# Optimization experiments

Hardware: AMD Instinct MI355X
Metric: run time of the kernel (lower is better)

## Reference

```python
import jax, jax.numpy as jnp
import numpy as np

NP, NR, NK = 64, 8, 500          # problems, rollouts, candidate nodes
H, HEADS, VD = 256, 8, 8         # hidden_dim, heads, vars_dim
HD = H // HEADS                  # head_dim
CLIP = 10.0                      # tanh logit clipping
NEG_INF = -jnp.inf


def setup_inputs() -> dict:
    key = jax.random.key(0)
    ks = jax.random.split(key, 17)
    f = lambda k, s: jax.random.normal(k, s, dtype=jnp.float32)
    B = NP * NR
    s = 1.0 / np.sqrt(H)
    return {
        "X": f(ks[0], (NP, NK, H)),
        "K": f(ks[1], (HEADS, NP, NK, HD)),
        "V": f(ks[2], (HEADS, NP, NK, HD)),
        "query": f(ks[3], (B, H)),
        "state1": f(ks[4], (B, H)),
        "state2": f(ks[5], (B, H)),
        "varfeat": f(ks[6], (NP, VD, NK)),
        "mask": jax.random.uniform(ks[7], (NP, NR, NK)) < 0.1,
        "nn_Q": f(ks[8], (HEADS, H, HD)) * (1.0 / np.sqrt(HD)),
        "nn_O": f(ks[9], (H, H)) * s,
        "nn_A": f(ks[10], (VD, H)) * s,
        "nn_B": f(ks[11], (H,)) * s,
        "nn_W": f(ks[12], (H,)) * s,
        "W_ih": f(ks[13], (4 * H, H)) * s,
        "W_hh": f(ks[14], (4 * H, H)) * s,
        "b_ih": f(ks[15], (4 * H,)) * s,
        "b_hh": f(ks[16], (4 * H,)) * s,
    }


def _decode(X, K, V, query, state1, state2, varfeat, mask,
            nn_Q, nn_O, nn_A, nn_B, nn_W, W_ih, W_hh, b_ih, b_hh):
    B = query.shape[0]
    # --- LSTMCell (PyTorch gate order: i, f, g, o) ---
    gates = query @ W_ih.T + b_ih + state1 @ W_hh.T + b_hh
    i, fg, g, o = jnp.split(gates, 4, axis=1)
    c = jax.nn.sigmoid(fg) * state2 + jax.nn.sigmoid(i) * jnp.tanh(g)
    h = jax.nn.sigmoid(o) * jnp.tanh(c)
    # --- MultiHeadAttention (glimpse) ---
    q = h.reshape(NP, NR, H)
    Q = jnp.einsum('pqh,ahd->apqd', q, nn_Q)                    # [heads,NP,NR,HD]
    S = jnp.einsum('apqd,apkd->apqk', Q, K) * (1.0 / np.sqrt(HD))
    S = jnp.where(mask[None], NEG_INF, S)
    S = jax.nn.softmax(S, axis=-1)
    x = jnp.einsum('apqk,apkd->apqd', S, V)
    x = x.transpose(1, 2, 0, 3).reshape(NP, NR, H)              # [NP,NR,H]
    qm = x @ nn_O                                               # glimpse query
    # --- additive attention with variable features ---
    vf = jnp.einsum('pvk,vh->pkh', varfeat, nn_A) + nn_B        # [NP,NK,H]
    t = jnp.tanh(X[:, None] + vf[:, None] + qm[:, :, None])     # [NP,NR,NK,H]
    logit = jnp.einsum('pqkh,h->pqk', t, nn_W)
    logit = jnp.where(mask, NEG_INF, logit).reshape(B, NK)
    # --- choose (mode=1: greedy argmax) ---
    infeasible = logit == NEG_INF
    l = jnp.where(infeasible, NEG_INF, jnp.tanh(logit) * CLIP)
    chosen = jnp.argmax(l, axis=1)
    logp = jax.nn.log_softmax(l, axis=1)
    chosen_p = jnp.take_along_axis(logp, chosen[:, None], axis=1).squeeze(1)
    return h, c, chosen_p


def reference(X, K, V, query, state1, state2, varfeat, mask,
              nn_Q, nn_O, nn_A, nn_B, nn_W, W_ih, W_hh, b_ih, b_hh):
    return _decode(X, K, V, query, state1, state2, varfeat, mask,
                   nn_Q, nn_O, nn_A, nn_B, nn_W, W_ih, W_hh, b_ih, b_hh)
```

## Files before the change

kernel.cpp:

```cpp
#include <hip/hip_runtime.h>

#define NPP   64
#define NRR   8
#define NKK   500
#define HDIM  256
#define NHEAD 8
#define VDIM  8
#define HD    32
#define BTOT  512

__device__ __forceinline__ float fast_tanh(float x) {
  const float e = __expf(2.f * x);
  return 1.f - 2.f * __builtin_amdgcn_rcpf(e + 1.f);
}
__device__ __forceinline__ float fast_sig(float x) {
  return __builtin_amdgcn_rcpf(1.f + __expf(-x));
}

__global__ __launch_bounds__(64) void k_lstm4(
    const float* __restrict__ query, const float* __restrict__ state1,
    const float* __restrict__ state2,
    const float* __restrict__ W_ih, const float* __restrict__ W_hh,
    const float* __restrict__ b_ih, const float* __restrict__ b_hh,
    const unsigned char* __restrict__ maskb, int* __restrict__ flagp,
    float* __restrict__ out_h, float* __restrict__ out_c)
{
  __shared__ float Wt[32][40];
  __shared__ float At[32][40];
  __shared__ float gt[32][40];

  const int t  = threadIdx.x;
  const int hb = blockIdx.x;
  const int bb = blockIdx.y;

  if (flagp != nullptr && hb == 0 && bb == 0) {
    __shared__ int f;
    if (t == 0) f = 0;
    __syncthreads();
    int any = 0;
    for (int j = t; j < 2048; j += 64) any |= maskb[2 * j + 1];
    if (any) atomicOr(&f, 1);
    __syncthreads();
    if (t == 0) *flagp = f;
  }

  const int tr = t >> 3, tc = t & 7;
  const int srow = t >> 1, sseg = (t & 1) * 16;
  const int wgrow = (srow >> 3) * HDIM + hb * 8 + (srow & 7);
  const int agrow = bb * 32 + srow;

  float acc[4][4];
#pragma unroll
  for (int i = 0; i < 4; ++i)
#pragma unroll
    for (int j = 0; j < 4; ++j) acc[i][j] = 0.f;

  for (int k0 = 0; k0 < 512; k0 += 32) {
    __syncthreads();
    {
      const float* wsrc = (k0 < 256) ? (W_ih + (size_t)wgrow * HDIM + k0)
                                     : (W_hh + (size_t)wgrow * HDIM + (k0 - 256));
      const float* asrc = (k0 < 256) ? (query  + (size_t)agrow * HDIM + k0)
                                     : (state1 + (size_t)agrow * HDIM + (k0 - 256));
#pragma unroll
      for (int j = 0; j < 4; ++j) {
        const float4 wv = *reinterpret_cast<const float4*>(wsrc + sseg + 4 * j);
        const float4 av = *reinterpret_cast<const float4*>(asrc + sseg + 4 * j);
        const int kk = sseg + 4 * j;
        Wt[kk + 0][srow] = wv.x; Wt[kk + 1][srow] = wv.y;
        Wt[kk + 2][srow] = wv.z; Wt[kk + 3][srow] = wv.w;
        At[kk + 0][srow] = av.x; At[kk + 1][srow] = av.y;
        At[kk + 2][srow] = av.z; At[kk + 3][srow] = av.w;
      }
    }
    __syncthreads();
#pragma unroll 8
    for (int kk = 0; kk < 32; ++kk) {
      const float4 wv = *reinterpret_cast<const float4*>(&Wt[kk][tr * 4]);
      const float4 av = *reinterpret_cast<const float4*>(&At[kk][tc * 4]);
      const float w[4] = {wv.x, wv.y, wv.z, wv.w};
      const float a[4] = {av.x, av.y, av.z, av.w};
#pragma unroll
      for (int i = 0; i < 4; ++i)
#pragma unroll
        for (int j = 0; j < 4; ++j) acc[i][j] += w[i] * a[j];
    }
  }

#pragma unroll
  for (int i = 0; i < 4; ++i) {
    float4 v;
    v.x = acc[i][0]; v.y = acc[i][1]; v.z = acc[i][2]; v.w = acc[i][3];
    *reinterpret_cast<float4*>(&gt[tr * 4 + i][tc * 4]) = v;
  }
  __syncthreads();

#pragma unroll
  for (int it = 0; it < 4; ++it) {
    const int cell = t + 64 * it;
    const int b = cell & 31, h = cell >> 5;
    const int gh = hb * 8 + h;
    const int gb = bb * 32 + b;
    const float bi = b_ih[0 * HDIM + gh] + b_hh[0 * HDIM + gh];
    const float bf = b_ih[1 * HDIM + gh] + b_hh[1 * HDIM + gh];
    const float bg = b_ih[2 * HDIM + gh] + b_hh[2 * HDIM + gh];
    const float bo = b_ih[3 * HDIM + gh] + b_hh[3 * HDIM + gh];
    const float iv = fast_sig (gt[ 0 + h][b] + bi);
    const float fv = fast_sig (gt[ 8 + h][b] + bf);
    const float gv = fast_tanh(gt[16 + h][b] + bg);
    const float ov = fast_sig (gt[24 + h][b] + bo);
    const size_t off = (size_t)gb * HDIM + gh;
    const float c = fv * state2[off] + iv * gv;
    out_c[off] = c;
    out_h[off] = ov * fast_tanh(c);
  }
}

__global__ __launch_bounds__(512, 4) void k_attn8(
    const float* __restrict__ Kt, const float* __restrict__ Vt,
    const float* __restrict__ nn_Q, const float* __restrict__ nn_O,
    const void* __restrict__ maskp, const int* __restrict__ flagp,
    const float* __restrict__ out_h, float* __restrict__ qm_slabs)
{
  const int p = blockIdx.x >> 3;
  const int a = blockIdx.x & 7;
  const int t = threadIdx.x;
  const int wave = t >> 6, lane = t & 63;

  __shared__ float hs[NRR][HDIM];
  __shared__ float Qs[NRR][36];
  __shared__ float Sb[NRR][512];
  __shared__ float pb[16][NRR][HD];
  __shared__ float xs[NRR][36];

  const float4 hv = reinterpret_cast<const float4*>(
      out_h + (size_t)p * NRR * HDIM)[t];

  const int flag = *flagp;

  const int kc = (t < NKK) ? t : (NKK - 1);
  const float4* kp4 = reinterpret_cast<const float4*>(
      Kt + (((size_t)a * NPP + p) * NKK + kc) * HD);
  float4 kreg[8];
#pragma unroll
  for (int j = 0; j < 8; ++j) kreg[j] = kp4[j];

  const int dpv = t & 31, kb = t >> 5;
  const float* vb = Vt + (((size_t)a * NPP + p) * NKK + (size_t)kb * 32) * HD + dpv;
  float vreg[32];
#pragma unroll
  for (int j = 0; j < 32; ++j)
    vreg[j] = (kb * 32 + j < NKK) ? vb[(size_t)j * HD] : 0.f;

  float maskv[NRR];
  {
    const unsigned char* mb = (const unsigned char*)maskp;
    const int* mi = (const int*)maskp;
#pragma unroll
    for (int r = 0; r < NRR; ++r) {
      const size_t mo = (size_t)(p * NRR + r) * NKK + kc;
      const bool mk = flag ? (mb[mo] != 0) : (mi[mo] != 0);
      maskv[r] = mk ? -INFINITY : 0.f;
    }
  }

  reinterpret_cast<float4*>(&hs[0][0])[t] = hv;
  __syncthreads();

  {
    const int r = wave, d4 = lane >> 3, ks = lane & 7;
    const float* qb = nn_Q + ((size_t)a * HDIM + ks * 32) * HD + d4 * 4;
    float qx = 0.f, qy = 0.f, qz = 0.f, qw = 0.f;
#pragma unroll
    for (int h = 0; h < 32; ++h) {
      const float hval = hs[r][ks * 32 + h];
      const float4 wv = *reinterpret_cast<const float4*>(qb + (size_t)h * HD);
      qx += hval * wv.x; qy += hval * wv.y;
      qz += hval * wv.z; qw += hval * wv.w;
    }
#pragma unroll
    for (int off = 1; off < 8; off <<= 1) {
      qx += __shfl_xor(qx, off, 64);
      qy += __shfl_xor(qy, off, 64);
      qz += __shfl_xor(qz, off, 64);
      qw += __shfl_xor(qw, off, 64);
    }
    if (ks == 0) {
      const float sc = 0.17677669529663687f;
      Qs[r][d4 * 4 + 0] = qx * sc; Qs[r][d4 * 4 + 1] = qy * sc;
      Qs[r][d4 * 4 + 2] = qz * sc; Qs[r][d4 * 4 + 3] = qw * sc;
    }
  }
  __syncthreads();

#pragma unroll
  for (int r = 0; r < NRR; ++r) {
    float s = 0.f;
#pragma unroll
    for (int j = 0; j < 8; ++j) {
      const float4 q = *reinterpret_cast<const float4*>(&Qs[r][j * 4]);
      const float4 k4 = kreg[j];
      s += q.x * k4.x + q.y * k4.y + q.z * k4.z + q.w * k4.w;
    }
    Sb[r][t] = (t < NKK) ? (s + maskv[r]) : -INFINITY;
  }
  __syncthreads();

  {
    const int r = wave;
    float lv[8], m = -INFINITY;
#pragma unroll
    for (int i = 0; i < 8; ++i) {
      lv[i] = Sb[r][lane + 64 * i];
      m = fmaxf(m, lv[i]);
    }
#pragma unroll
    for (int off = 32; off > 0; off >>= 1) m = fmaxf(m, __shfl_xor(m, off, 64));
    float ssum = 0.f;
#pragma unroll
    for (int i = 0; i < 8; ++i) {
      lv[i] = __expf(lv[i] - m);
      ssum += lv[i];
    }
#pragma unroll
    for (int off = 32; off > 0; off >>= 1) ssum += __shfl_xor(ssum, off, 64);
    const float inv = 1.f / ssum;
#pragma unroll
    for (int i = 0; i < 8; ++i) Sb[r][lane + 64 * i] = lv[i] * inv;
  }
  __syncthreads();

  {
    float acc[NRR];
#pragma unroll
    for (int r = 0; r < NRR; ++r) acc[r] = 0.f;
#pragma unroll
    for (int j4 = 0; j4 < 8; ++j4) {
      const float v0 = vreg[j4 * 4 + 0], v1 = vreg[j4 * 4 + 1];
      const float v2 = vreg[j4 * 4 + 2], v3 = vreg[j4 * 4 + 3];
#pragma unroll
      for (int r = 0; r < NRR; ++r) {
        const float4 s4 = *reinterpret_cast<const float4*>(
            &Sb[r][kb * 32 + j4 * 4]);
        acc[r] += s4.x * v0 + s4.y * v1 + s4.z * v2 + s4.w * v3;
      }
    }
#pragma unroll
    for (int r = 0; r < NRR; ++r) pb[kb][r][dpv] = acc[r];
  }
  __syncthreads();

  if (t < 256) {
    const int r = t >> 5, d = t & 31;
    float s = 0.f;
#pragma unroll
    for (int q = 0; q < 16; ++q) s += pb[q][r][d];
    xs[r][d] = s;
  }
  __syncthreads();

  {
    const int j = t & 255, rr = t >> 8;
    float a0 = 0.f, a1 = 0.f, a2 = 0.f, a3 = 0.f;
#pragma unroll
    for (int d4 = 0; d4 < 8; ++d4) {
      const float4 x0 = *reinterpret_cast<const float4*>(&xs[rr * 4 + 0][d4 * 4]);
      const float4 x1 = *reinterpret_cast<const float4*>(&xs[rr * 4 + 1][d4 * 4]);
      const float4 x2 = *reinterpret_cast<const float4*>(&xs[rr * 4 + 2][d4 * 4]);
      const float4 x3 = *reinterpret_cast<const float4*>(&xs[rr * 4 + 3][d4 * 4]);
      const float c0[4] = {x0.x, x0.y, x0.z, x0.w};
      const float c1[4] = {x1.x, x1.y, x1.z, x1.w};
      const float c2[4] = {x2.x, x2.y, x2.z, x2.w};
      const float c3[4] = {x3.x, x3.y, x3.z, x3.w};
#pragma unroll
      for (int dd = 0; dd < 4; ++dd) {
        const float w = nn_O[((size_t)(a * HD + d4 * 4 + dd)) * HDIM + j];
        a0 += c0[dd] * w; a1 += c1[dd] * w;
        a2 += c2[dd] * w; a3 += c3[dd] * w;
      }
    }
    float* slab = qm_slabs + (size_t)a * BTOT * HDIM;
    slab[(size_t)(p * NRR + rr * 4 + 0) * HDIM + j] = a0;
    slab[(size_t)(p * NRR + rr * 4 + 1) * HDIM + j] = a1;
    slab[(size_t)(p * NRR + rr * 4 + 2) * HDIM + j] = a2;
    slab[(size_t)(p * NRR + rr * 4 + 3) * HDIM + j] = a3;
  }
}

__global__ __launch_bounds__(256) void k_logits6(
    const float* __restrict__ X, const float* __restrict__ varfeat,
    const float* __restrict__ nn_A, const float* __restrict__ nn_B,
    const float* __restrict__ nn_W, const float* __restrict__ qm_slabs,
    const int* __restrict__ flagp, const void* __restrict__ maskp,
    float* __restrict__ pmax, float* __restrict__ psum)
{
  const int p  = blockIdx.x >> 5;
  const int kt = blockIdx.x & 31;
  const int t = threadIdx.x;
  const int wave = t >> 6, lane = t & 63;
  const int h0 = lane * 4;

  __shared__ float qb[NRR][260];
  __shared__ float red[4][NRR][2];

  const unsigned char* mb = (const unsigned char*)maskp;
  const int* mi = (const int*)maskp;
  const int flag = *flagp;
  const bool mbyte = (flag != 0);

  for (int s = t; s < 512; s += 256) {
    const int r = s >> 6, h4 = s & 63;
    const float4 bv = *reinterpret_cast<const float4*>(nn_B + h4 * 4);
    float qx = bv.x, qy = bv.y, qz = bv.z, qw = bv.w;
#pragma unroll
    for (int a = 0; a < NHEAD; ++a) {
      const float4 q = *reinterpret_cast<const float4*>(
          qm_slabs + (size_t)a * BTOT * HDIM +
          (size_t)(p * NRR + r) * HDIM + h4 * 4);
      qx += q.x; qy += q.y; qz += q.z; qw += q.w;
    }
    qb[r][h4 * 4 + 0] = qx; qb[r][h4 * 4 + 1] = qy;
    qb[r][h4 * 4 + 2] = qz; qb[r][h4 * 4 + 3] = qw;
  }
  __syncthreads();

  const float4 w4 = *reinterpret_cast<const float4*>(nn_W + h0);
  float4 a4r[VDIM];
#pragma unroll
  for (int v = 0; v < VDIM; ++v)
    a4r[v] = *reinterpret_cast<const float4*>(nn_A + (size_t)v * HDIM + h0);
  float4 q4r[NRR];
#pragma unroll
  for (int r = 0; r < NRR; ++r)
    q4r[r] = *reinterpret_cast<const float4*>(&qb[r][h0]);

  float rmax = -INFINITY, rsum = 0.f;

  for (int kk = 0; kk < 4; ++kk) {
    const int k = kt * 16 + wave * 4 + kk;
    if (k >= NKK) break;

    const float4 x4 = *reinterpret_cast<const float4*>(
        X + ((size_t)p * NKK + k) * HDIM + h0);
    float base0 = x4.x, base1 = x4.y, base2 = x4.z, base3 = x4.w;
#pragma unroll
    for (int v = 0; v < VDIM; ++v) {
      const float vv = varfeat[((size_t)p * VDIM + v) * NKK + k];
      base0 += vv * a4r[v].x; base1 += vv * a4r[v].y;
      base2 += vv * a4r[v].z; base3 += vv * a4r[v].w;
    }

    float acc[NRR];
#pragma unroll
    for (int r = 0; r < NRR; ++r) {
      acc[r] = fast_tanh(base0 + q4r[r].x) * w4.x
             + fast_tanh(base1 + q4r[r].y) * w4.y
             + fast_tanh(base2 + q4r[r].z) * w4.z
             + fast_tanh(base3 + q4r[r].w) * w4.w;
    }

    float v4[4];
    {
      float sw[8];
#pragma unroll
      for (int j = 0; j < 8; ++j) sw[j] = __shfl_xor(acc[j], 32, 64);
      const bool hi = (lane & 32) != 0;
#pragma unroll
      for (int j = 0; j < 4; ++j)
        v4[j] = hi ? (acc[j + 4] + sw[j + 4]) : (acc[j] + sw[j]);
    }
    float v2[2];
    {
      float sw[4];
#pragma unroll
      for (int j = 0; j < 4; ++j) sw[j] = __shfl_xor(v4[j], 16, 64);
      const bool hi = (lane & 16) != 0;
      v2[0] = hi ? (v4[2] + sw[2]) : (v4[0] + sw[0]);
      v2[1] = hi ? (v4[3] + sw[3]) : (v4[1] + sw[1]);
    }
    float w;
    {
      const float s0 = __shfl_xor(v2[0], 8, 64);
      const float s1 = __shfl_xor(v2[1], 8, 64);
      w = ((lane & 8) != 0) ? (v2[1] + s1) : (v2[0] + s0);
    }
    w += __shfl_xor(w, 4, 64);
    w += __shfl_xor(w, 2, 64);
    w += __shfl_xor(w, 1, 64);

    if ((lane & 7) == 0) {
      const int r = lane >> 3;
      const size_t mrow = (size_t)(p * NRR + r) * NKK + k;
      const bool mk = mbyte ? (mb[mrow] != 0) : (mi[mrow] != 0);
      const float l = mk ? -INFINITY : fast_tanh(w) * 10.0f;
      rmax = fmaxf(rmax, l);
      rsum += __expf(l - 10.f);
    }
  }

  if ((lane & 7) == 0) {
    red[wave][lane >> 3][0] = rmax;
    red[wave][lane >> 3][1] = rsum;
  }
  __syncthreads();
  if (t < NRR) {
    float m = red[0][t][0], s = red[0][t][1];
#pragma unroll
    for (int w = 1; w < 4; ++w) {
      m = fmaxf(m, red[w][t][0]);
      s += red[w][t][1];
    }
    pmax[(size_t)(p * NRR + t) * 32 + kt] = m;
    psum[(size_t)(p * NRR + t) * 32 + kt] = s;
  }
}

__global__ __launch_bounds__(64) void k_choose2(
    const float* __restrict__ pmax, const float* __restrict__ psum,
    float* __restrict__ out_p)
{
  const int b = blockIdx.x;
  const int lane = threadIdx.x;
  float m = (lane < 32) ? pmax[(size_t)b * 32 + lane] : -INFINITY;
  float s = (lane < 32) ? psum[(size_t)b * 32 + lane] : 0.f;
#pragma unroll
  for (int off = 16; off > 0; off >>= 1) {
    m = fmaxf(m, __shfl_xor(m, off, 64));
    s += __shfl_xor(s, off, 64);
  }
  if (lane == 0) out_p[b] = m - 10.f - logf(s);
}

__global__ __launch_bounds__(256) void k_fused(
    const float* __restrict__ X, const float* __restrict__ Kt,
    const float* __restrict__ Vt, const float* __restrict__ varfeat,
    const void* __restrict__ maskp,
    const float* __restrict__ nn_Q, const float* __restrict__ nn_O,
    const float* __restrict__ nn_A, const float* __restrict__ nn_B,
    const float* __restrict__ nn_W,
    const float* __restrict__ out_h, float* __restrict__ out_p)
{
  const int p = blockIdx.x >> 3;
  const int r = blockIdx.x & 7;
  const int t = threadIdx.x;
  const int wave = t >> 6, lane = t & 63;

  __shared__ float hs[HDIM];
  __shared__ float Qs[NHEAD][HD];
  __shared__ float Sb[NHEAD][NKK];
  __shared__ float xs[HDIM];
  __shared__ float qs[HDIM];
  __shared__ float As2[HDIM][VDIM];
  __shared__ float Ws[HDIM];
  __shared__ float lsb[NKK];
  __shared__ int   mask_any;

  const unsigned char* mb = (const unsigned char*)maskp;
  if (t == 0) mask_any = 0;
  __syncthreads();
  {
    int any = 0;
    for (int j = t; j < 2048; j += 256) any |= mb[2 * j + 1];
    if (any) atomicOr(&mask_any, 1);
  }
  for (int idx = t; idx < VDIM * HDIM; idx += 256)
    As2[idx & 255][idx >> 8] = nn_A[idx];
  Ws[t] = nn_W[t];
  hs[t] = out_h[(size_t)(p * NRR + r) * HDIM + t];
  __syncthreads();
  const bool mbyte = (mask_any != 0);
  const int* mi = (const int*)maskp;
  const size_t mrow = (size_t)(p * NRR + r) * NKK;
  {
    const int a = t >> 5, d = t & 31;
    const float* nq = nn_Q + (size_t)a * HDIM * HD + d;
    float acc = 0.f;
    for (int h = 0; h < HDIM; ++h) acc += hs[h] * nq[(size_t)h * HD];
    Qs[a][d] = acc * 0.17677669529663687f;
  }
  __syncthreads();
  for (int k = t; k < NKK; k += 256) {
    const bool mk = mbyte ? (mb[mrow + k] != 0) : (mi[mrow + k] != 0);
#pragma unroll
    for (int a = 0; a < NHEAD; ++a) {
      const float4* kr4 = reinterpret_cast<const float4*>(
          Kt + (((size_t)a * NPP + p) * NKK + k) * HD);
      float s = 0.f;
#pragma unroll
      for (int d4 = 0; d4 < HD / 4; ++d4) {
        const float4 u = kr4[d4];
        s += Qs[a][4 * d4] * u.x + Qs[a][4 * d4 + 1] * u.y
           + Qs[a][4 * d4 + 2] * u.z + Qs[a][4 * d4 + 3] * u.w;
      }
      Sb[a][k] = mk ? -INFINITY : s;
    }
  }
  __syncthreads();
  for (int aa = 0; aa < 2; ++aa) {
    const int a = wave * 2 + aa;
    float m = -INFINITY;
    for (int k = lane; k < NKK; k += 64) m = fmaxf(m, Sb[a][k]);
#pragma unroll
    for (int off = 32; off > 0; off >>= 1) m = fmaxf(m, __shfl_xor(m, off, 64));
    float ssum = 0.f;
    for (int k = lane; k < NKK; k += 64) {
      const float e = expf(Sb[a][k] - m);
      Sb[a][k] = e; ssum += e;
    }
#pragma unroll
    for (int off = 32; off > 0; off >>= 1) ssum += __shfl_xor(ssum, off, 64);
    const float inv = 1.f / ssum;
    for (int k = lane; k < NKK; k += 64) Sb[a][k] *= inv;
  }
  __syncthreads();
  {
    const int a = t >> 5, d = t & 31;
    const float* vb = Vt + ((size_t)a * NPP + p) * NKK * HD + d;
    float acc = 0.f;
    for (int k = 0; k < NKK; ++k) acc += Sb[a][k] * vb[(size_t)k * HD];
    xs[a * HD + d] = acc;
  }
  __syncthreads();
  {
    float acc = 0.f;
    for (int i = 0; i < HDIM; ++i) acc += xs[i] * nn_O[(size_t)i * HDIM + t];
    qs[t] = acc + nn_B[t];
  }
  __syncthreads();
  for (int k = t; k < NKK; k += 256) {
    float vfv[VDIM];
#pragma unroll
    for (int v = 0; v < VDIM; ++v)
      vfv[v] = varfeat[((size_t)p * VDIM + v) * NKK + k];
    const float4* xp4 = reinterpret_cast<const float4*>(
        X + ((size_t)p * NKK + k) * HDIM);
    float acc = 0.f;
    for (int h4 = 0; h4 < HDIM / 4; ++h4) {
      const float4 ux = xp4[h4];
      const float xv[4] = {ux.x, ux.y, ux.z, ux.w};
#pragma unroll
      for (int j = 0; j < 4; ++j) {
        const int h = 4 * h4 + j;
        float base = xv[j] + qs[h];
        const float4 a0 = *reinterpret_cast<const float4*>(&As2[h][0]);
        const float4 a1 = *reinterpret_cast<const float4*>(&As2[h][4]);
        base += vfv[0] * a0.x + vfv[1] * a0.y + vfv[2] * a0.z + vfv[3] * a0.w
              + vfv[4] * a1.x + vfv[5] * a1.y + vfv[6] * a1.z + vfv[7] * a1.w;
        acc += tanhf(base) * Ws[h];
      }
    }
    lsb[k] = acc;
  }
  __syncthreads();
  for (int k = t; k < NKK; k += 256) {
    const bool mk = mbyte ? (mb[mrow + k] != 0) : (mi[mrow + k] != 0);
    lsb[k] = mk ? -INFINITY : tanhf(lsb[k]) * 10.0f;
  }
  __syncthreads();
  if (wave == 0) {
    float m = -INFINITY;
    for (int k = lane; k < NKK; k += 64) m = fmaxf(m, lsb[k]);
#pragma unroll
    for (int off = 32; off > 0; off >>= 1) m = fmaxf(m, __shfl_xor(m, off, 64));
    float s = 0.f;
    for (int k = lane; k < NKK; k += 64) s += expf(lsb[k] - m);
#pragma unroll
    for (int off = 32; off > 0; off >>= 1) s += __shfl_xor(s, off, 64);
    if (lane == 0) out_p[p * NRR + r] = -logf(s);
  }
}

extern "C" void kernel_launch(void* const* d_in, const int* in_sizes, int n_in,
                              void* d_out, int out_size, void* d_ws, size_t ws_size,
                              hipStream_t stream)
{
  const float* X       = (const float*)d_in[0];
  const float* Kt      = (const float*)d_in[1];
  const float* Vt      = (const float*)d_in[2];
  const float* query   = (const float*)d_in[3];
  const float* state1  = (const float*)d_in[4];
  const float* state2  = (const float*)d_in[5];
  const float* varfeat = (const float*)d_in[6];
  const void*  maskp   = d_in[7];
  const float* nn_Q    = (const float*)d_in[8];
  const float* nn_O    = (const float*)d_in[9];
  const float* nn_A    = (const float*)d_in[10];
  const float* nn_B    = (const float*)d_in[11];
  const float* nn_W    = (const float*)d_in[12];
  const float* W_ih    = (const float*)d_in[13];
  const float* W_hh    = (const float*)d_in[14];
  const float* b_ih    = (const float*)d_in[15];
  const float* b_hh    = (const float*)d_in[16];

  float* out   = (float*)d_out;
  float* out_h = out;
  float* out_c = out + (size_t)BTOT * HDIM;
  float* out_p = out + (size_t)2 * BTOT * HDIM;

  const size_t flag_bytes = 256;
  const size_t qm8_bytes  = (size_t)NHEAD * BTOT * HDIM * 4;
  const size_t part_bytes = (size_t)BTOT * 32 * 4;
  const size_t need = flag_bytes + qm8_bytes + 2 * part_bytes;

  if (ws_size >= need) {
    int*   flagp = (int*)d_ws;
    float* qmw  = (float*)((char*)d_ws + flag_bytes);
    float* pmax = (float*)((char*)d_ws + flag_bytes + qm8_bytes);
    float* psum = (float*)((char*)d_ws + flag_bytes + qm8_bytes + part_bytes);

    hipLaunchKernelGGL(k_lstm4, dim3(32, 16), dim3(64), 0, stream,
                       query, state1, state2, W_ih, W_hh, b_ih, b_hh,
                       (const unsigned char*)maskp, flagp, out_h, out_c);
    hipLaunchKernelGGL(k_attn8, dim3(NPP * NHEAD), dim3(512), 0, stream,
                       Kt, Vt, nn_Q, nn_O, maskp, flagp, out_h, qmw);
    hipLaunchKernelGGL(k_logits6, dim3(NPP * 32), dim3(256), 0, stream,
                       X, varfeat, nn_A, nn_B, nn_W, qmw, flagp, maskp,
                       pmax, psum);
    hipLaunchKernelGGL(k_choose2, dim3(BTOT), dim3(64), 0, stream,
                       pmax, psum, out_p);
  } else {
    hipLaunchKernelGGL(k_lstm4, dim3(32, 16), dim3(64), 0, stream,
                       query, state1, state2, W_ih, W_hh, b_ih, b_hh,
                       (const unsigned char*)maskp, nullptr, out_h, out_c);
    hipLaunchKernelGGL(k_fused, dim3(NPP * NRR), dim3(256), 0, stream,
                       X, Kt, Vt, varfeat, maskp,
                       nn_Q, nn_O, nn_A, nn_B, nn_W,
                       out_h, out_p);
  }
}
```

Before: 234.9 us.

## Retile LSTM GEMM with prefetch, restructure PV in attention, split qm reduction

```diff
diff --git a/kernel.cpp b/kernel.cpp
--- a/kernel.cpp
+++ b/kernel.cpp
@@ -17,7 +17,7 @@
   return __builtin_amdgcn_rcpf(1.f + __expf(-x));
 }
 
-__global__ __launch_bounds__(64) void k_lstm4(
+__global__ __launch_bounds__(128) void k_lstm5(
     const float* __restrict__ query, const float* __restrict__ state1,
     const float* __restrict__ state2,
     const float* __restrict__ W_ih, const float* __restrict__ W_hh,
@@ -25,9 +25,9 @@
     const unsigned char* __restrict__ maskb, int* __restrict__ flagp,
     float* __restrict__ out_h, float* __restrict__ out_c)
 {
-  __shared__ float Wt[32][40];
-  __shared__ float At[32][40];
-  __shared__ float gt[32][40];
+  __shared__ float Wt[32][36];
+  __shared__ float At[32][68];
+  __shared__ float gt[32][68];
 
   const int t  = threadIdx.x;
   const int hb = blockIdx.x;
@@ -38,16 +38,61 @@
     if (t == 0) f = 0;
     __syncthreads();
     int any = 0;
-    for (int j = t; j < 2048; j += 64) any |= maskb[2 * j + 1];
+    for (int j = t; j < 2048; j += 128) any |= maskb[2 * j + 1];
     if (any) atomicOr(&f, 1);
     __syncthreads();
     if (t == 0) *flagp = f;
   }
 
-  const int tr = t >> 3, tc = t & 7;
-  const int srow = t >> 1, sseg = (t & 1) * 16;
-  const int wgrow = (srow >> 3) * HDIM + hb * 8 + (srow & 7);
-  const int agrow = bb * 32 + srow;
+  const int tr = t >> 4;
+  const int tc = t & 15;
+
+  const int grow = t >> 2;
+  const int kseg = t & 3;
+  const int wgrow = (grow >> 3) * HDIM + hb * 8 + (grow & 7);
+  const int agrow0 = bb * 64 + grow;
+  const int agrow1 = agrow0 + 32;
+
+  float4 wr0, wr1, ar0, ar1, ar2, ar3;
+
+#define LSTM_ISSUE(K0)                                                        \
+  {                                                                           \
+    const int k0_ = (K0);                                                     \
+    const float* wsrc = (k0_ < 256)                                           \
+        ? (W_ih + (size_t)wgrow * HDIM + k0_)                                 \
+        : (W_hh + (size_t)wgrow * HDIM + (k0_ - 256));                        \
+    wr0 = *reinterpret_cast<const float4*>(wsrc + kseg * 8);                  \
+    wr1 = *reinterpret_cast<const float4*>(wsrc + kseg * 8 + 4);              \
+    const float* asrc0 = (k0_ < 256)                                          \
+        ? (query  + (size_t)agrow0 * HDIM + k0_)                              \
+        : (state1 + (size_t)agrow0 * HDIM + (k0_ - 256));                     \
+    ar0 = *reinterpret_cast<const float4*>(asrc0 + kseg * 8);                 \
+    ar1 = *reinterpret_cast<const float4*>(asrc0 + kseg * 8 + 4);             \
+    const float* asrc1 = (k0_ < 256)                                          \
+        ? (query  + (size_t)agrow1 * HDIM + k0_)                              \
+        : (state1 + (size_t)agrow1 * HDIM + (k0_ - 256));                     \
+    ar2 = *reinterpret_cast<const float4*>(asrc1 + kseg * 8);                 \
+    ar3 = *reinterpret_cast<const float4*>(asrc1 + kseg * 8 + 4);             \
+  }
+
+#define LSTM_WRITE()                                                          \
+  {                                                                           \
+    const float w0[4] = {wr0.x, wr0.y, wr0.z, wr0.w};                         \
+    const float w1[4] = {wr1.x, wr1.y, wr1.z, wr1.w};                         \
+    const float a0[4] = {ar0.x, ar0.y, ar0.z, ar0.w};                         \
+    const float a1[4] = {ar1.x, ar1.y, ar1.z, ar1.w};                         \
+    const float a2[4] = {ar2.x, ar2.y, ar2.z, ar2.w};                         \
+    const float a3[4] = {ar3.x, ar3.y, ar3.z, ar3.w};                         \
+    _Pragma("unroll")                                                         \
+    for (int i = 0; i < 4; ++i) {                                             \
+      Wt[kseg * 8 + i][grow]     = w0[i];                                     \
+      Wt[kseg * 8 + 4 + i][grow] = w1[i];                                     \
+      At[kseg * 8 + i][grow]     = a0[i];                                     \
+      At[kseg * 8 + 4 + i][grow] = a1[i];                                     \
+      At[kseg * 8 + i][grow + 32]     = a2[i];                                \
+      At[kseg * 8 + 4 + i][grow + 32] = a3[i];                                \
+    }                                                                         \
+  }
 
   float acc[4][4];
 #pragma unroll
@@ -55,25 +100,14 @@
 #pragma unroll
     for (int j = 0; j < 4; ++j) acc[i][j] = 0.f;
 
+  LSTM_ISSUE(0);
+  LSTM_WRITE();
+  __syncthreads();
+
   for (int k0 = 0; k0 < 512; k0 += 32) {
-    __syncthreads();
-    {
-      const float* wsrc = (k0 < 256) ? (W_ih + (size_t)wgrow * HDIM + k0)
-                                     : (W_hh + (size_t)wgrow * HDIM + (k0 - 256));
-      const float* asrc = (k0 < 256) ? (query  + (size_t)agrow * HDIM + k0)
-                                     : (state1 + (size_t)agrow * HDIM + (k0 - 256));
-#pragma unroll
-      for (int j = 0; j < 4; ++j) {
-        const float4 wv = *reinterpret_cast<const float4*>(wsrc + sseg + 4 * j);
-        const float4 av = *reinterpret_cast<const float4*>(asrc + sseg + 4 * j);
-        const int kk = sseg + 4 * j;
-        Wt[kk + 0][srow] = wv.x; Wt[kk + 1][srow] = wv.y;
-        Wt[kk + 2][srow] = wv.z; Wt[kk + 3][srow] = wv.w;
-        At[kk + 0][srow] = av.x; At[kk + 1][srow] = av.y;
-        At[kk + 2][srow] = av.z; At[kk + 3][srow] = av.w;
-      }
-    }
-    __syncthreads();
+    const bool more = (k0 + 32) < 512;
+    if (more) LSTM_ISSUE(k0 + 32);
+
 #pragma unroll 8
     for (int kk = 0; kk < 32; ++kk) {
       const float4 wv = *reinterpret_cast<const float4*>(&Wt[kk][tr * 4]);
@@ -85,6 +119,11 @@
 #pragma unroll
         for (int j = 0; j < 4; ++j) acc[i][j] += w[i] * a[j];
     }
+    __syncthreads();
+    if (more) {
+      LSTM_WRITE();
+      __syncthreads();
+    }
   }
 
 #pragma unroll
@@ -97,10 +136,10 @@
 
 #pragma unroll
   for (int it = 0; it < 4; ++it) {
-    const int cell = t + 64 * it;
-    const int b = cell & 31, h = cell >> 5;
+    const int cell = t + 128 * it;
+    const int h = cell & 7, b = cell >> 3;
     const int gh = hb * 8 + h;
-    const int gb = bb * 32 + b;
+    const int gb = bb * 64 + b;
     const float bi = b_ih[0 * HDIM + gh] + b_hh[0 * HDIM + gh];
     const float bf = b_ih[1 * HDIM + gh] + b_hh[1 * HDIM + gh];
     const float bg = b_ih[2 * HDIM + gh] + b_hh[2 * HDIM + gh];
@@ -116,7 +155,7 @@
   }
 }
 
-__global__ __launch_bounds__(512, 4) void k_attn8(
+__global__ __launch_bounds__(512) void k_attn10(
     const float* __restrict__ Kt, const float* __restrict__ Vt,
     const float* __restrict__ nn_Q, const float* __restrict__ nn_O,
     const void* __restrict__ maskp, const int* __restrict__ flagp,
@@ -130,7 +169,7 @@
   __shared__ float hs[NRR][HDIM];
   __shared__ float Qs[NRR][36];
   __shared__ float Sb[NRR][512];
-  __shared__ float pb[16][NRR][HD];
+  __shared__ float pb[8][NRR][HD];
   __shared__ float xs[NRR][36];
 
   const float4 hv = reinterpret_cast<const float4*>(
@@ -145,13 +184,6 @@
 #pragma unroll
   for (int j = 0; j < 8; ++j) kreg[j] = kp4[j];
 
-  const int dpv = t & 31, kb = t >> 5;
-  const float* vb = Vt + (((size_t)a * NPP + p) * NKK + (size_t)kb * 32) * HD + dpv;
-  float vreg[32];
-#pragma unroll
-  for (int j = 0; j < 32; ++j)
-    vreg[j] = (kb * 32 + j < NKK) ? vb[(size_t)j * HD] : 0.f;
-
   float maskv[NRR];
   {
     const unsigned char* mb = (const unsigned char*)maskp;
@@ -168,15 +200,21 @@
   __syncthreads();
 
   {
-    const int r = wave, d4 = lane >> 3, ks = lane & 7;
-    const float* qb = nn_Q + ((size_t)a * HDIM + ks * 32) * HD + d4 * 4;
+    const int r = wave;
+    const int d4 = lane >> 3, ks = lane & 7;
     float qx = 0.f, qy = 0.f, qz = 0.f, qw = 0.f;
 #pragma unroll
-    for (int h = 0; h < 32; ++h) {
-      const float hval = hs[r][ks * 32 + h];
-      const float4 wv = *reinterpret_cast<const float4*>(qb + (size_t)h * HD);
-      qx += hval * wv.x; qy += hval * wv.y;
-      qz += hval * wv.z; qw += hval * wv.w;
+    for (int i = 0; i < 8; ++i) {
+      const int hb = 32 * i + ks * 4;
+      const float4 hv4 = *reinterpret_cast<const float4*>(&hs[r][hb]);
+      const float hh[4] = {hv4.x, hv4.y, hv4.z, hv4.w};
+      const float* nqb = nn_Q + ((size_t)a * HDIM + hb) * HD + d4 * 4;
+#pragma unroll
+      for (int jj = 0; jj < 4; ++jj) {
+        const float4 wv = *reinterpret_cast<const float4*>(nqb + (size_t)jj * HD);
+        qx += hh[jj] * wv.x; qy += hh[jj] * wv.y;
+        qz += hh[jj] * wv.z; qw += hh[jj] * wv.w;
+      }
     }
 #pragma unroll
     for (int off = 1; off < 8; off <<= 1) {
@@ -204,6 +242,20 @@
     }
     Sb[r][t] = (t < NKK) ? (s + maskv[r]) : -INFINITY;
   }
+
+  const int kg = t >> 3;
+  const int d4p = t & 7;
+  float4 v4[8];
+  {
+    const float* vbase = Vt + ((size_t)a * NPP + p) * NKK * HD + d4p * 4;
+#pragma unroll
+    for (int j = 0; j < 8; ++j) {
+      const int k = kg + 64 * j;
+      v4[j] = (k < NKK)
+          ? *reinterpret_cast<const float4*>(vbase + (size_t)k * HD)
+          : make_float4(0.f, 0.f, 0.f, 0.f);
+    }
+  }
   __syncthreads();
 
   {
@@ -231,22 +283,34 @@
   __syncthreads();
 
   {
-    float acc[NRR];
-#pragma unroll
-    for (int r = 0; r < NRR; ++r) acc[r] = 0.f;
-#pragma unroll
-    for (int j4 = 0; j4 < 8; ++j4) {
-      const float v0 = vreg[j4 * 4 + 0], v1 = vreg[j4 * 4 + 1];
-      const float v2 = vreg[j4 * 4 + 2], v3 = vreg[j4 * 4 + 3];
+    float4 acc4[NRR];
+#pragma unroll
+    for (int r = 0; r < NRR; ++r) acc4[r] = make_float4(0.f, 0.f, 0.f, 0.f);
+#pragma unroll
+    for (int j = 0; j < 8; ++j) {
+      const float4 v = v4[j];
 #pragma unroll
       for (int r = 0; r < NRR; ++r) {
-        const float4 s4 = *reinterpret_cast<const float4*>(
-            &Sb[r][kb * 32 + j4 * 4]);
-        acc[r] += s4.x * v0 + s4.y * v1 + s4.z * v2 + s4.w * v3;
+        const float s = Sb[r][kg + 64 * j];
+        acc4[r].x += s * v.x; acc4[r].y += s * v.y;
+        acc4[r].z += s * v.z; acc4[r].w += s * v.w;
       }
     }
 #pragma unroll
-    for (int r = 0; r < NRR; ++r) pb[kb][r][dpv] = acc[r];
+    for (int off = 8; off < 64; off <<= 1) {
+#pragma unroll
+      for (int r = 0; r < NRR; ++r) {
+        acc4[r].x += __shfl_xor(acc4[r].x, off, 64);
+        acc4[r].y += __shfl_xor(acc4[r].y, off, 64);
+        acc4[r].z += __shfl_xor(acc4[r].z, off, 64);
+        acc4[r].w += __shfl_xor(acc4[r].w, off, 64);
+      }
+    }
+    if (lane < 8) {
+#pragma unroll
+      for (int r = 0; r < NRR; ++r)
+        *reinterpret_cast<float4*>(&pb[wave][r][lane * 4]) = acc4[r];
+    }
   }
   __syncthreads();
 
@@ -254,7 +318,7 @@
     const int r = t >> 5, d = t & 31;
     float s = 0.f;
 #pragma unroll
-    for (int q = 0; q < 16; ++q) s += pb[q][r][d];
+    for (int w = 0; w < 8; ++w) s += pb[w][r][d];
     xs[r][d] = s;
   }
   __syncthreads();
@@ -287,10 +351,26 @@
   }
 }
 
-__global__ __launch_bounds__(256) void k_logits6(
+__global__ __launch_bounds__(256) void k_qsum(
+    const float* __restrict__ qm_slabs, const float* __restrict__ nn_B,
+    float* __restrict__ qbg)
+{
+  const int idx = blockIdx.x * 256 + threadIdx.x;
+  const int row = idx >> 6, h4 = idx & 63;
+  float4 acc = *reinterpret_cast<const float4*>(nn_B + h4 * 4);
+#pragma unroll
+  for (int a = 0; a < NHEAD; ++a) {
+    const float4 q = *reinterpret_cast<const float4*>(
+        qm_slabs + (size_t)a * BTOT * HDIM + (size_t)row * HDIM + h4 * 4);
+    acc.x += q.x; acc.y += q.y; acc.z += q.z; acc.w += q.w;
+  }
+  *reinterpret_cast<float4*>(qbg + (size_t)row * HDIM + h4 * 4) = acc;
+}
+
+__global__ __launch_bounds__(256) void k_logits7(
     const float* __restrict__ X, const float* __restrict__ varfeat,
-    const float* __restrict__ nn_A, const float* __restrict__ nn_B,
-    const float* __restrict__ nn_W, const float* __restrict__ qm_slabs,
+    const float* __restrict__ nn_A, const float* __restrict__ nn_W,
+    const float* __restrict__ qbg,
     const int* __restrict__ flagp, const void* __restrict__ maskp,
     float* __restrict__ pmax, float* __restrict__ psum)
 {
@@ -300,7 +380,6 @@
   const int wave = t >> 6, lane = t & 63;
   const int h0 = lane * 4;
 
-  __shared__ float qb[NRR][260];
   __shared__ float red[4][NRR][2];
 
   const unsigned char* mb = (const unsigned char*)maskp;
@@ -308,22 +387,6 @@
   const int flag = *flagp;
   const bool mbyte = (flag != 0);
 
-  for (int s = t; s < 512; s += 256) {
-    const int r = s >> 6, h4 = s & 63;
-    const float4 bv = *reinterpret_cast<const float4*>(nn_B + h4 * 4);
-    float qx = bv.x, qy = bv.y, qz = bv.z, qw = bv.w;
-#pragma unroll
-    for (int a = 0; a < NHEAD; ++a) {
-      const float4 q = *reinterpret_cast<const float4*>(
-          qm_slabs + (size_t)a * BTOT * HDIM +
-          (size_t)(p * NRR + r) * HDIM + h4 * 4);
-      qx += q.x; qy += q.y; qz += q.z; qw += q.w;
-    }
-    qb[r][h4 * 4 + 0] = qx; qb[r][h4 * 4 + 1] = qy;
-    qb[r][h4 * 4 + 2] = qz; qb[r][h4 * 4 + 3] = qw;
-  }
-  __syncthreads();
-
   const float4 w4 = *reinterpret_cast<const float4*>(nn_W + h0);
   float4 a4r[VDIM];
 #pragma unroll
@@ -332,7 +395,8 @@
   float4 q4r[NRR];
 #pragma unroll
   for (int r = 0; r < NRR; ++r)
-    q4r[r] = *reinterpret_cast<const float4*>(&qb[r][h0]);
+    q4r[r] = *reinterpret_cast<const float4*>(
+        qbg + (size_t)(p * NRR + r) * HDIM + h0);
 
   float rmax = -INFINITY, rsum = 0.f;
 
@@ -599,27 +663,32 @@
 
   const size_t flag_bytes = 256;
   const size_t qm8_bytes  = (size_t)NHEAD * BTOT * HDIM * 4;
+  const size_t qbg_bytes  = (size_t)BTOT * HDIM * 4;
   const size_t part_bytes = (size_t)BTOT * 32 * 4;
-  const size_t need = flag_bytes + qm8_bytes + 2 * part_bytes;
+  const size_t need = flag_bytes + qm8_bytes + qbg_bytes + 2 * part_bytes;
 
   if (ws_size >= need) {
     int*   flagp = (int*)d_ws;
     float* qmw  = (float*)((char*)d_ws + flag_bytes);
-    float* pmax = (float*)((char*)d_ws + flag_bytes + qm8_bytes);
-    float* psum = (float*)((char*)d_ws + flag_bytes + qm8_bytes + part_bytes);
-
-    hipLaunchKernelGGL(k_lstm4, dim3(32, 16), dim3(64), 0, stream,
+    float* qbg  = (float*)((char*)d_ws + flag_bytes + qm8_bytes);
+    float* pmax = (float*)((char*)d_ws + flag_bytes + qm8_bytes + qbg_bytes);
+    float* psum = (float*)((char*)d_ws + flag_bytes + qm8_bytes + qbg_bytes
+                           + part_bytes);
+
+    hipLaunchKernelGGL(k_lstm5, dim3(32, 8), dim3(128), 0, stream,
                        query, state1, state2, W_ih, W_hh, b_ih, b_hh,
                        (const unsigned char*)maskp, flagp, out_h, out_c);
-    hipLaunchKernelGGL(k_attn8, dim3(NPP * NHEAD), dim3(512), 0, stream,
+    hipLaunchKernelGGL(k_attn10, dim3(NPP * NHEAD), dim3(512), 0, stream,
                        Kt, Vt, nn_Q, nn_O, maskp, flagp, out_h, qmw);
-    hipLaunchKernelGGL(k_logits6, dim3(NPP * 32), dim3(256), 0, stream,
-                       X, varfeat, nn_A, nn_B, nn_W, qmw, flagp, maskp,
+    hipLaunchKernelGGL(k_qsum, dim3(128), dim3(256), 0, stream,
+                       qmw, nn_B, qbg);
+    hipLaunchKernelGGL(k_logits7, dim3(NPP * 32), dim3(256), 0, stream,
+                       X, varfeat, nn_A, nn_W, qbg, flagp, maskp,
                        pmax, psum);
     hipLaunchKernelGGL(k_choose2, dim3(BTOT), dim3(64), 0, stream,
                        pmax, psum, out_p);
   } else {
-    hipLaunchKernelGGL(k_lstm4, dim3(32, 16), dim3(64), 0, stream,
+    hipLaunchKernelGGL(k_lstm5, dim3(32, 8), dim3(128), 0, stream,
                        query, state1, state2, W_ih, W_hh, b_ih, b_hh,
                        (const unsigned char*)maskp, nullptr, out_h, out_c);
     hipLaunchKernelGGL(k_fused, dim3(NPP * NRR), dim3(256), 0, stream,
```

After: 227.1 us. 1.03x faster.
